# Kernel optimization log

Measured on AMD Instinct MI355X. Metric: run time of the kernel, lower is better.

## Reference

```python
import jax, jax.numpy as jnp
import numpy as np
from jax import lax

VOCAB = 400000
D = 300          # embedding_dim
L = 2000         # seq len
B = 4            # batch
C1, K1 = 64, 3   # conv1 outChan, kernel
C2, K2 = 128, 500
HID = 256
NCLS = 5


def setup_inputs() -> dict:
    key = jax.random.key(0)
    ks = jax.random.split(key, 8)
    x = jax.random.randint(ks[0], (B, L), 0, VOCAB)
    emb_table = jax.random.normal(ks[1], (VOCAB, D), jnp.float32) * 0.1
    conv1_w = jax.random.normal(ks[2], (C1, 1, K1), jnp.float32) * 0.1
    conv1_b = jnp.zeros((C1,), jnp.float32)
    conv2_w = jax.random.normal(ks[3], (C2, C1, K2), jnp.float32) * 0.02
    conv2_b = jnp.zeros((C2,), jnp.float32)
    lin1_w = jax.random.normal(ks[4], (HID, C2), jnp.float32) * 0.05
    lin1_b = jnp.zeros((HID,), jnp.float32)
    lin2_w = jax.random.normal(ks[5], (NCLS, HID), jnp.float32) * 0.05
    lin2_b = jnp.zeros((NCLS,), jnp.float32)
    return dict(x=x, emb_table=emb_table,
                conv1_w=conv1_w, conv1_b=conv1_b,
                conv2_w=conv2_w, conv2_b=conv2_b,
                lin1_w=lin1_w, lin1_b=lin1_b,
                lin2_w=lin2_w, lin2_b=lin2_b)


def _conv1d(x, w):
    # x: [N, Cin, W]; w: [Cout, Cin, K]; VALID, stride 1
    return lax.conv_general_dilated(x, w, window_strides=(1,), padding='VALID',
                                    dimension_numbers=('NCH', 'OIH', 'NCH'))


def _maxpool1d(x, k):
    # kernel == stride (torch MaxPool1d default)
    return lax.reduce_window(x, -jnp.inf, lax.max, (1, 1, k), (1, 1, k), 'VALID')


def reference(x, emb_table, conv1_w, conv1_b, conv2_w, conv2_b,
              lin1_w, lin1_b, lin2_w, lin2_b):
    emb = emb_table[x]                                  # [B, L, D]
    # concat module == reshape to [B, 1, L*D]
    out = emb.reshape(emb.shape[0], 1, emb.shape[1] * emb.shape[2])
    out = _conv1d(out, conv1_w) + conv1_b[None, :, None]  # [B, C1, L*D-K1+1]
    out = _maxpool1d(jax.nn.relu(out), D)                 # pool 300
    out = _conv1d(out, conv2_w) + conv2_b[None, :, None]  # [B, C2, 1500]
    out = _maxpool1d(jax.nn.relu(out), D * 5)             # pool 1500 -> len 1
    out = out.reshape(out.shape[0], -1)                   # [B, C2]
    out = jax.nn.relu(out @ lin1_w.T + lin1_b)            # [B, HID]
    out = jax.nn.softmax(out @ lin2_w.T + lin2_b, axis=-1)  # [B, 5]
    # Dropout is identity in eval mode
    return out
```

## Files before the change

### kernel.cpp

```cpp
#include <hip/hip_runtime.h>
#include <hip/hip_bf16.h>
#include <math.h>

#define VOCAB 400000
#define D     300
#define L     2000
#define B     4
#define C1    64
#define C2    128
#define K2    500
#define HID   256
#define NCLS  5
#define NP1   1999
#define T2    1500
#define TPAD  2304
#define S     8
#define CI    8
#define NK2   125
#define BN    96
#define SEGR  640
#define NWT   128
#define NC1B  (B * 500)

typedef __attribute__((ext_vector_type(8))) short short8v;
typedef __attribute__((ext_vector_type(4))) float f32x4;

__device__ __forceinline__ void gload_lds16(const void* g, void* l) {
    __builtin_amdgcn_global_load_lds(
        (const __attribute__((address_space(1))) void*)g,
        (__attribute__((address_space(3))) void*)l, 16, 0, 0);
}

__global__ __launch_bounds__(256) void k_prep(
    const int* __restrict__ x, const float* __restrict__ emb,
    const float* __restrict__ w1, const float* __restrict__ b1,
    const float* __restrict__ w2,
    __hip_bfloat16* __restrict__ in1T, __hip_bfloat16* __restrict__ aT)
{
    __shared__ float smem[1204];
    int bid = blockIdx.x, tid = threadIdx.x;
    if (bid < NWT) {
        int s = bid >> 4, cog = bid & 15;
        for (int u = tid; u < 4000; u += 256) {
            int co_l = u & 7, kg = u >> 3;
            int k2 = kg >> 2, g = kg & 3;
            int co = cog * 8 + co_l;
            __hip_bfloat16 tmp[8];
#pragma unroll
            for (int e = 0; e < 8; ++e)
                tmp[e] = __float2bfloat16(
                    w2[((size_t)co * C1 + s * CI + e) * K2 + 4 * k2 + g]);
            *reinterpret_cast<int4*>(
                aT + ((size_t)((s * NK2 + k2) * 4 + g)) * 1024 + (size_t)co * 8) =
                *reinterpret_cast<const int4*>(tmp);
        }
    } else {
        int blk = bid - NWT;
        int b = blk / 500, pb = blk % 500;
        int p0 = pb * 4;
        float* sig = smem;
        for (int i = tid; i < 301; i += 256) {
            int rj = i / 75, col = (i % 75) * 4;
            int xi = p0 + rj; if (xi > L - 1) xi = L - 1;
            int row = x[b * L + xi];
            *reinterpret_cast<float4*>(sig + 4 * i) =
                *reinterpret_cast<const float4*>(emb + (size_t)row * D + col);
        }
        __syncthreads();
        int c = tid & 63, pg = tid >> 6;
        int p = p0 + pg;
        float wa = w1[c * 3 + 0], wb = w1[c * 3 + 1], wc = w1[c * 3 + 2];
        float bb = b1[c];
        int jb = 300 * pg;
        float m = -INFINITY;
        float4 cur = *reinterpret_cast<float4*>(sig + jb);
        for (int st = 0; st < 75; ++st) {
            float4 nxt = *reinterpret_cast<float4*>(sig + jb + 4 * st + 4);
            float xx[8] = {cur.x, cur.y, cur.z, cur.w, nxt.x, nxt.y, nxt.z, nxt.w};
#pragma unroll
            for (int q = 0; q < 4; ++q) {
                float v = fmaf(wc, xx[q + 2], fmaf(wb, xx[q + 1], fmaf(wa, xx[q], bb)));
                m = fmaxf(m, v);
            }
            cur = nxt;
        }
        if (p < NP1) {
            int sg = c >> 3, ci = c & 7;
            in1T[((size_t)(b * S + sg) * TPAD + p) * CI + ci] =
                __float2bfloat16(fmaxf(m, 0.0f));
        }
    }
}

__global__ __launch_bounds__(256, 2) void k2_mfma(
    const __hip_bfloat16* __restrict__ in1T,
    const __hip_bfloat16* __restrict__ aT,
    float* __restrict__ part)
{
    int bid = blockIdx.x;
    int s = bid & 7;
    int rem = bid >> 3;
    int b = rem >> 4, ti = rem & 15;
    int t0 = ti * BN;

    __shared__ __align__(16) __hip_bfloat16 seg[SEGR * CI];

    int tid = threadIdx.x;
    int w = tid >> 6, l = tid & 63;
    int lane16 = l & 15, g = l >> 4;
    int co0w = (w & 1) * 64;
    int tn0  = (w >> 1) * 48;

    {
        const char* gsrc = (const char*)(in1T + ((size_t)(b * S + s) * TPAD + t0) * CI);
        char* lb = (char*)seg + w * 1024;
        gload_lds16(gsrc + (size_t)tid * 16, lb);
        gload_lds16(gsrc + (size_t)(256 + tid) * 16, lb + 4096);
        if (tid < 128)
            gload_lds16(gsrc + (size_t)(512 + tid) * 16, lb + 8192);
    }
    __syncthreads();

    const __hip_bfloat16* abase =
        aT + (size_t)s * NK2 * 4096 + g * 1024 + (co0w + lane16) * 8;

    f32x4 acc[4][3];
#pragma unroll
    for (int fa = 0; fa < 4; ++fa)
#pragma unroll
        for (int fb = 0; fb < 3; ++fb) acc[fa][fb] = (f32x4){0.f, 0.f, 0.f, 0.f};

#define LOADA(AR, KK)                                                         \
    {                                                                         \
        _Pragma("unroll")                                                     \
        for (int fa = 0; fa < 4; ++fa)                                        \
            AR[fa] = *reinterpret_cast<const short8v*>(                       \
                abase + (size_t)(KK) * 4096 + fa * 128);                      \
    }

#define STEP(AR, KK)                                                         \
    {                                                                         \
        short8v bfr[3];                                                       \
        _Pragma("unroll")                                                     \
        for (int fb = 0; fb < 3; ++fb)                                        \
            bfr[fb] = *reinterpret_cast<const short8v*>(                      \
                seg + (size_t)(tn0 + fb * 16 + lane16 + 4 * (KK) + g) * 8);   \
        __builtin_amdgcn_s_setprio(1);                                        \
        _Pragma("unroll")                                                     \
        for (int fa = 0; fa < 4; ++fa) {                                      \
            _Pragma("unroll")                                                 \
            for (int fb = 0; fb < 3; ++fb)                                    \
                acc[fa][fb] = __builtin_amdgcn_mfma_f32_16x16x32_bf16(        \
                    AR[fa], bfr[fb], acc[fa][fb], 0, 0, 0);                   \
        }                                                                     \
        __builtin_amdgcn_s_setprio(0);                                        \
    }

    short8v a0[4], a1[4];
    LOADA(a0, 0);
    LOADA(a1, 1);
    int k2 = 0;
#pragma unroll 1
    for (; k2 + 3 < NK2; k2 += 2) {
        STEP(a0, k2);
        LOADA(a0, k2 + 2);
        STEP(a1, k2 + 1);
        LOADA(a1, k2 + 3);
    }
    STEP(a0, k2);
    LOADA(a0, k2 + 2);
    STEP(a1, k2 + 1);
    STEP(a0, k2 + 2);

#undef LOADA
#undef STEP

#pragma unroll
    for (int fa = 0; fa < 4; ++fa) {
#pragma unroll
        for (int fb = 0; fb < 3; ++fb) {
            int t = t0 + tn0 + fb * 16 + lane16;
            if (t < T2) {
                int cob = co0w + fa * 16 + 4 * g;
#pragma unroll
                for (int r = 0; r < 4; ++r)
                    part[((size_t)(s * B + b) * C2 + cob + r) * T2 + t] =
                        acc[fa][fb][r];
            }
        }
    }
}

__global__ __launch_bounds__(256) void k2b_pool(
    const float* __restrict__ part, const float* __restrict__ b2,
    float* __restrict__ h1)
{
    int bc = blockIdx.x;
    int b = bc / C2, co = bc % C2;
    int tid = threadIdx.x;
    float m = -INFINITY;
    for (int t4 = tid; t4 < T2 / 4; t4 += 256) {
        float4 sum = {0.f, 0.f, 0.f, 0.f};
#pragma unroll
        for (int s = 0; s < S; ++s) {
            const float4* p = reinterpret_cast<const float4*>(
                part + ((size_t)(s * B + b) * C2 + co) * T2);
            float4 v = p[t4];
            sum.x += v.x; sum.y += v.y; sum.z += v.z; sum.w += v.w;
        }
        m = fmaxf(m, fmaxf(fmaxf(sum.x, sum.y), fmaxf(sum.z, sum.w)));
    }
    __shared__ float red[256];
    red[tid] = m;
    __syncthreads();
    for (int st = 128; st > 0; st >>= 1) {
        if (tid < st) red[tid] = fmaxf(red[tid], red[tid + st]);
        __syncthreads();
    }
    if (tid == 0) h1[bc] = fmaxf(red[0] + b2[co], 0.0f);
}

__global__ __launch_bounds__(256) void k3_head(
    const float* __restrict__ h1,
    const float* __restrict__ wl1, const float* __restrict__ bl1,
    const float* __restrict__ wl2, const float* __restrict__ bl2,
    float* __restrict__ out)
{
    int b = blockIdx.x;
    int tid = threadIdx.x;
    __shared__ float xin[C2];
    __shared__ float hbuf[HID];
    __shared__ float lg[NCLS];
    if (tid < C2) xin[tid] = h1[b * C2 + tid];
    __syncthreads();
    float a = bl1[tid];
    for (int c = 0; c < C2; ++c) a = fmaf(xin[c], wl1[tid * C2 + c], a);
    hbuf[tid] = fmaxf(a, 0.0f);
    __syncthreads();
    if (tid < NCLS) {
        float lv = bl2[tid];
        for (int j = 0; j < HID; ++j) lv = fmaf(hbuf[j], wl2[tid * HID + j], lv);
        lg[tid] = lv;
    }
    __syncthreads();
    if (tid < NCLS) {
        float mx = lg[0];
        for (int i = 1; i < NCLS; ++i) mx = fmaxf(mx, lg[i]);
        float sum = 0.f;
        for (int i = 0; i < NCLS; ++i) sum += expf(lg[i] - mx);
        out[b * NCLS + tid] = expf(lg[tid] - mx) / sum;
    }
}

extern "C" void kernel_launch(void* const* d_in, const int* in_sizes, int n_in,
                              void* d_out, int out_size, void* d_ws, size_t ws_size,
                              hipStream_t stream)
{
    const int*   x   = (const int*)  d_in[0];
    const float* emb = (const float*)d_in[1];
    const float* w1  = (const float*)d_in[2];
    const float* b1  = (const float*)d_in[3];
    const float* w2  = (const float*)d_in[4];
    const float* b2  = (const float*)d_in[5];
    const float* wl1 = (const float*)d_in[6];
    const float* bl1 = (const float*)d_in[7];
    const float* wl2 = (const float*)d_in[8];
    const float* bl2 = (const float*)d_in[9];
    float* out = (float*)d_out;

    float* ws   = (float*)d_ws;
    float* part = ws;
    float* h1   = ws + (size_t)S * B * C2 * T2;
    __hip_bfloat16* in1T = (__hip_bfloat16*)(h1 + 512);
    __hip_bfloat16* aT   = in1T + (size_t)B * S * TPAD * CI;

    hipLaunchKernelGGL(k_prep, dim3(NWT + NC1B), dim3(256), 0, stream,
                       x, emb, w1, b1, w2, in1T, aT);
    hipLaunchKernelGGL(k2_mfma, dim3(512), dim3(256), 0, stream, in1T, aT, part);
    hipLaunchKernelGGL(k2b_pool, dim3(B * C2), dim3(256), 0, stream, part, b2, h1);
    hipLaunchKernelGGL(k3_head, dim3(B), dim3(256), 0, stream,
                       h1, wl1, bl1, wl2, bl2, out);
}
```

Baseline: 78.51 us.

## Split conv2 blocks over output-channel halves and two input-channel slices each

Each k2_mfma block now covers two input-channel slices and half of the output channels, instead of one slice and all 128 channels. This halves the fp32 partial-sum buffer and the reads k2b_pool does to reduce it. The grid stays at 512 blocks. In exchange, each block loads twice the LDS input segment, each wave holds fewer accumulators, and the same B tile is loaded by two blocks.

```diff
diff --git a/kernel.cpp b/kernel.cpp
--- a/kernel.cpp
+++ b/kernel.cpp
@@ -15,6 +15,7 @@
 #define T2    1500
 #define TPAD  2304
 #define S     8
+#define SP    4
 #define CI    8
 #define NK2   125
 #define BN    96
@@ -98,56 +99,62 @@
     float* __restrict__ part)
 {
     int bid = blockIdx.x;
-    int s = bid & 7;
+    int spair = (bid >> 1) & 3;
+    int cog   = bid & 1;
     int rem = bid >> 3;
     int b = rem >> 4, ti = rem & 15;
     int t0 = ti * BN;
-
-    __shared__ __align__(16) __hip_bfloat16 seg[SEGR * CI];
+    int s0 = spair * 2;
+
+    __shared__ __align__(16) __hip_bfloat16 seg[2 * SEGR * CI];
 
     int tid = threadIdx.x;
     int w = tid >> 6, l = tid & 63;
     int lane16 = l & 15, g = l >> 4;
-    int co0w = (w & 1) * 64;
+    int co0w = cog * 64 + (w & 1) * 32;
     int tn0  = (w >> 1) * 48;
 
     {
-        const char* gsrc = (const char*)(in1T + ((size_t)(b * S + s) * TPAD + t0) * CI);
+        const char* g0 = (const char*)(in1T + ((size_t)(b * S + s0) * TPAD + t0) * CI);
+        const char* g1 = (const char*)(in1T + ((size_t)(b * S + s0 + 1) * TPAD + t0) * CI);
         char* lb = (char*)seg + w * 1024;
-        gload_lds16(gsrc + (size_t)tid * 16, lb);
-        gload_lds16(gsrc + (size_t)(256 + tid) * 16, lb + 4096);
-        if (tid < 128)
-            gload_lds16(gsrc + (size_t)(512 + tid) * 16, lb + 8192);
+#pragma unroll
+        for (int r = 0; r < 5; ++r) {
+            int u = r * 256 + tid;
+            const char* src = (u < SEGR) ? (g0 + (size_t)u * 16)
+                                         : (g1 + (size_t)(u - SEGR) * 16);
+            gload_lds16(src, lb + r * 4096);
+        }
     }
     __syncthreads();
 
     const __hip_bfloat16* abase =
-        aT + (size_t)s * NK2 * 4096 + g * 1024 + (co0w + lane16) * 8;
-
-    f32x4 acc[4][3];
-#pragma unroll
-    for (int fa = 0; fa < 4; ++fa)
+        aT + (size_t)s0 * NK2 * 4096 + g * 1024 + (co0w + lane16) * 8;
+
+    f32x4 acc[2][3];
+#pragma unroll
+    for (int fa = 0; fa < 2; ++fa)
 #pragma unroll
         for (int fb = 0; fb < 3; ++fb) acc[fa][fb] = (f32x4){0.f, 0.f, 0.f, 0.f};
 
-#define LOADA(AR, KK)                                                         \
+#define LOADA(AR, AB, KK)                                                     \
     {                                                                         \
         _Pragma("unroll")                                                     \
-        for (int fa = 0; fa < 4; ++fa)                                        \
+        for (int fa = 0; fa < 2; ++fa)                                        \
             AR[fa] = *reinterpret_cast<const short8v*>(                       \
-                abase + (size_t)(KK) * 4096 + fa * 128);                      \
-    }
-
-#define STEP(AR, KK)                                                         \
+                (AB) + (size_t)(KK) * 4096 + fa * 128);                       \
+    }
+
+#define STEP(AR, BB, KK)                                                      \
     {                                                                         \
         short8v bfr[3];                                                       \
         _Pragma("unroll")                                                     \
         for (int fb = 0; fb < 3; ++fb)                                        \
             bfr[fb] = *reinterpret_cast<const short8v*>(                      \
-                seg + (size_t)(tn0 + fb * 16 + lane16 + 4 * (KK) + g) * 8);   \
+                (BB) + (size_t)(tn0 + fb * 16 + lane16 + 4 * (KK) + g) * 8);  \
         __builtin_amdgcn_s_setprio(1);                                        \
         _Pragma("unroll")                                                     \
-        for (int fa = 0; fa < 4; ++fa) {                                      \
+        for (int fa = 0; fa < 2; ++fa) {                                      \
             _Pragma("unroll")                                                 \
             for (int fb = 0; fb < 3; ++fb)                                    \
                 acc[fa][fb] = __builtin_amdgcn_mfma_f32_16x16x32_bf16(        \
@@ -156,27 +163,32 @@
         __builtin_amdgcn_s_setprio(0);                                        \
     }
 
-    short8v a0[4], a1[4];
-    LOADA(a0, 0);
-    LOADA(a1, 1);
-    int k2 = 0;
 #pragma unroll 1
-    for (; k2 + 3 < NK2; k2 += 2) {
-        STEP(a0, k2);
-        LOADA(a0, k2 + 2);
-        STEP(a1, k2 + 1);
-        LOADA(a1, k2 + 3);
-    }
-    STEP(a0, k2);
-    LOADA(a0, k2 + 2);
-    STEP(a1, k2 + 1);
-    STEP(a0, k2 + 2);
+    for (int ph = 0; ph < 2; ++ph) {
+        const __hip_bfloat16* ab = abase + (size_t)ph * NK2 * 4096;
+        const __hip_bfloat16* bb = seg + (size_t)ph * SEGR * CI;
+        short8v a0[2], a1[2];
+        LOADA(a0, ab, 0);
+        LOADA(a1, ab, 1);
+        int k2 = 0;
+#pragma unroll 1
+        for (; k2 + 3 < NK2; k2 += 2) {
+            STEP(a0, bb, k2);
+            LOADA(a0, ab, k2 + 2);
+            STEP(a1, bb, k2 + 1);
+            LOADA(a1, ab, k2 + 3);
+        }
+        STEP(a0, bb, k2);
+        LOADA(a0, ab, k2 + 2);
+        STEP(a1, bb, k2 + 1);
+        STEP(a0, bb, k2 + 2);
+    }
 
 #undef LOADA
 #undef STEP
 
 #pragma unroll
-    for (int fa = 0; fa < 4; ++fa) {
+    for (int fa = 0; fa < 2; ++fa) {
 #pragma unroll
         for (int fb = 0; fb < 3; ++fb) {
             int t = t0 + tn0 + fb * 16 + lane16;
@@ -184,7 +196,7 @@
                 int cob = co0w + fa * 16 + 4 * g;
 #pragma unroll
                 for (int r = 0; r < 4; ++r)
-                    part[((size_t)(s * B + b) * C2 + cob + r) * T2 + t] =
+                    part[((size_t)(spair * B + b) * C2 + cob + r) * T2 + t] =
                         acc[fa][fb][r];
             }
         }
@@ -202,9 +214,9 @@
     for (int t4 = tid; t4 < T2 / 4; t4 += 256) {
         float4 sum = {0.f, 0.f, 0.f, 0.f};
 #pragma unroll
-        for (int s = 0; s < S; ++s) {
+        for (int sp = 0; sp < SP; ++sp) {
             const float4* p = reinterpret_cast<const float4*>(
-                part + ((size_t)(s * B + b) * C2 + co) * T2);
+                part + ((size_t)(sp * B + b) * C2 + co) * T2);
             float4 v = p[t4];
             sum.x += v.x; sum.y += v.y; sum.z += v.z; sum.w += v.w;
         }
@@ -270,7 +282,7 @@
 
     float* ws   = (float*)d_ws;
     float* part = ws;
-    float* h1   = ws + (size_t)S * B * C2 * T2;
+    float* h1   = ws + (size_t)SP * B * C2 * T2;
     __hip_bfloat16* in1T = (__hip_bfloat16*)(h1 + 512);
     __hip_bfloat16* aT   = in1T + (size_t)B * S * TPAD * CI;
 
```

New measurement: 81.61 us. 1.04x slower.
